# Kernel optimization log

Hardware: AMD Instinct MI355X
Metric: run time of the kernel (lower is better)

The kernel has to match this reference:

```python
import jax, jax.numpy as jnp
import numpy as np

N = 400_000
B = 64          # number of segments (point clouds)
IN_C = 128
INTER = (256, 512, 512)
OUT_C = 512


def setup_inputs() -> dict:
    key = jax.random.key(0)
    ks = jax.random.split(key, 12)
    pos_emd = jax.random.normal(ks[0], (N, IN_C), dtype=jnp.float32)
    radius_p_batch = jnp.sort(jax.random.randint(ks[1], (N,), 0, B))

    def lin(k, fin, fout):
        kw, kb = jax.random.split(k)
        s = 1.0 / np.sqrt(fin)
        W = jax.random.uniform(kw, (fin, fout), jnp.float32, -s, s)
        b = jax.random.uniform(kb, (fout,), jnp.float32, -s, s)
        return W, b

    W1, b1 = lin(ks[2], IN_C, INTER[0])
    W2, b2 = lin(ks[3], INTER[0], INTER[1])
    W3, b3 = lin(ks[4], INTER[1], INTER[2])
    W4, b4 = lin(ks[5], IN_C + INTER[2], OUT_C)
    W5, b5 = lin(ks[6], OUT_C, OUT_C)
    return {
        "pos_emd": pos_emd, "radius_p_batch": radius_p_batch,
        "W1": W1, "b1": b1, "W2": W2, "b2": b2, "W3": W3, "b3": b3,
        "W4": W4, "b4": b4, "W5": W5, "b5": b5,
    }


def reference(pos_emd, radius_p_batch, W1, b1, W2, b2, W3, b3, W4, b4, W5, b5):
    # mlp1: Linear-ReLU-Linear-ReLU-Linear
    h = jax.nn.relu(pos_emd @ W1 + b1)
    h = jax.nn.relu(h @ W2 + b2)
    h = h @ W3 + b3                              # [N, 512]
    # global max pool over segments
    g = jax.ops.segment_max(h, radius_p_batch, num_segments=B)  # [B, 512]
    # broadcast each segment's global feature back to its points (ids sorted)
    g_rep = g[radius_p_batch]                    # [N, 512]
    z = jnp.concatenate((pos_emd, g_rep), axis=-1)  # [N, 640]
    # mlp2: Linear-ReLU-Linear
    z = jax.nn.relu(z @ W4 + b4)
    z = z @ W5 + b5                              # [N, 512]
    return jax.ops.segment_max(z, radius_p_batch, num_segments=B)  # [B, 512]
```

## Files before the change

kernel.cpp:

```cpp
#include <hip/hip_runtime.h>
#include <stdint.h>


typedef __bf16 bf16;
typedef __bf16 bf16x4 __attribute__((ext_vector_type(4)));
typedef __bf16 bf16x8 __attribute__((ext_vector_type(8)));
typedef float f32x4 __attribute__((ext_vector_type(4)));
typedef __attribute__((address_space(3))) char lds_char;

#define N_PTS 400000
#define ORD_NEG_INF 0x007FFFFFu

__device__ __forceinline__ unsigned f2ord(float f) {
  unsigned u = __float_as_uint(f);
  return (u & 0x80000000u) ? ~u : (u | 0x80000000u);
}
__device__ __forceinline__ float ord2f(unsigned o) {
  unsigned u = (o & 0x80000000u) ? (o ^ 0x80000000u) : ~o;
  return __uint_as_float(u);
}

__device__ __forceinline__ void gld16(const bf16* g, lds_char* l) {
  __builtin_amdgcn_global_load_lds((const __attribute__((address_space(1))) void*)g,
                                   (__attribute__((address_space(3))) void*)l, 16, 0, 0);
}

#define DSR(dst, preg, IMM) \
  asm volatile("ds_read_b128 %0, %1 offset:%c2" : "=&v"(dst) : "v"(preg), "n"(IMM))

#define SCHED0 __builtin_amdgcn_sched_barrier(0)
#define LGKM0 do { asm volatile("s_waitcnt lgkmcnt(0)"); SCHED0; } while (0)
#define SBARR do { __builtin_amdgcn_s_barrier(); SCHED0; } while (0)
#define VMW2 do { asm volatile("s_waitcnt vmcnt(2)"); SCHED0; } while (0)
#define VMW0 do { asm volatile("s_waitcnt vmcnt(0)"); SCHED0; } while (0)

__global__ void k_init(unsigned* g_ord, unsigned* out_u) {
  int i = blockIdx.x * 256 + threadIdx.x;
  if (i < 64 * 512) { g_ord[i] = ORD_NEG_INF; out_u[i] = ORD_NEG_INF; }
}

__global__ void k_convX(const float* __restrict__ x, bf16* __restrict__ y, long n4) {
  long i = (long)blockIdx.x * 256 + threadIdx.x;
  long stride = (long)gridDim.x * 256;
  for (; i < n4; i += stride) {
    float4 v = ((const float4*)x)[i];
    bf16x4 o = {(bf16)v.x, (bf16)v.y, (bf16)v.z, (bf16)v.w};
    ((bf16x4*)y)[i] = o;
  }
}

__global__ void k_convWt(const float* __restrict__ W, bf16* __restrict__ Wt, int K, int Nout) {
  int idx = blockIdx.x * 256 + threadIdx.x;
  if (idx < K * Nout) {
    int k = idx / Nout, c = idx - k * Nout;
    Wt[(size_t)c * K + k] = (bf16)W[idx];
  }
}

__global__ void k_segbias(const unsigned* __restrict__ g_ord, const float* __restrict__ W4,
                          const float* __restrict__ b4, float* __restrict__ sb) {
  const int s = blockIdx.x, c = threadIdx.x;
  __shared__ float gs[512];
  gs[c] = ord2f(g_ord[s * 512 + c]);
  __syncthreads();
  float acc = b4[c];
  for (int j = 0; j < 512; ++j) acc = fmaf(gs[j], W4[(size_t)(128 + j) * 512 + c], acc);
  sb[s * 512 + c] = acc;
}

__global__ void k_decode(unsigned* p, int n) {
  int i = blockIdx.x * 256 + threadIdx.x;
  if (i < n) { float f = ord2f(p[i]); ((float*)p)[i] = f; }
}

template <int BIASMODE, bool RELU, int EPI, int K, int NOUT>
__launch_bounds__(512, 1)
__global__ void k_gemm(const bf16* __restrict__ A, const bf16* __restrict__ Bt,
                       const float* __restrict__ bias, const int* __restrict__ ids,
                       long row_off, bf16* __restrict__ out,
                       unsigned* __restrict__ outAtomic) {
  constexpr int NT = K / 64;
  constexpr int NIT = NT / 2;
  constexpr int NBX = NOUT / 256;
  __shared__ __align__(16) char sMem[131072];
  __shared__ int sIds[256];
  const int tid = threadIdx.x;
  const int wid = tid >> 6, lane = tid & 63;
  const int wr = wid >> 2, wc = wid & 3;
  const int lr = lane & 15, lk = lane >> 4;

  const int nwg = NBX * (int)gridDim.y;
  const int orig = (int)blockIdx.y * NBX + (int)blockIdx.x;
  const int q = nwg >> 3, r = nwg & 7;
  const int xcd = orig & 7, lid = orig >> 3;
  const int wg = (xcd < r ? xcd * (q + 1) : r * (q + 1) + (xcd - r) * q) + lid;
  const int n0 = (wg % NBX) * 256;
  const int m0 = (wg / NBX) * 256;

  if constexpr (BIASMODE == 1 || EPI == 1) {
    if (tid < 256) {
      long gi = row_off + m0 + tid;
      if (gi > (long)N_PTS - 1) gi = (long)N_PTS - 1;
      sIds[tid] = ids[gi];
    }
  }
  SCHED0;

  const int row0 = (wid * 2) * 8 + (lane >> 3);
  const int row1 = row0 + 8;
  const int sc0 = ((lane & 7) ^ (lane >> 4)) * 8;
  const int sc1 = ((lane & 7) ^ (4 + (lane >> 4))) * 8;
  lds_char* lds3 = (lds_char*)sMem;

  auto stageH = [&](int tau, int mat, int h) {
    if (tau >= NT) return;
    const int db = tau & 1;
    const bf16* srcb = (mat == 0) ? A + (size_t)(m0 + h * 128) * K
                                  : Bt + (size_t)(n0 + h * 128) * K;
    lds_char* d0 = lds3 + mat * 65536 + h * 32768 + db * 16384 + (wid * 2) * 1024;
    gld16(srcb + (size_t)row0 * K + tau * 64 + sc0, d0);
    gld16(srcb + (size_t)row1 * K + tau * 64 + sc1, d0 + 1024);
  };

  const unsigned s7 = (unsigned)(lr >> 1);
  const unsigned cks0 = (((unsigned)lk) ^ s7) * 16u;
  const unsigned cks1 = (((unsigned)lk + 4u) ^ s7) * 16u;
  lds_char* vA0 = lds3 + wr * 32768 + lr * 128 + cks0;
  lds_char* vA1 = lds3 + wr * 32768 + lr * 128 + cks1;
  lds_char* vB0 = lds3 + 65536 + (wc >> 1) * 32768 + (wc & 1) * 8192 + lr * 128 + cks0;
  lds_char* vB1 = lds3 + 65536 + (wc >> 1) * 32768 + (wc & 1) * 8192 + lr * 128 + cks1;

  bf16x8 aF[4][2], aS[4][2], bR[4][2];
  f32x4 acc[8][4];
#pragma unroll
  for (int i = 0; i < 8; ++i)
#pragma unroll
    for (int j = 0; j < 4; ++j) acc[i][j] = {0.f, 0.f, 0.f, 0.f};

#define RDA4(ARR, DB, IHI) do { \
  DSR(ARR[0][0], vA0, (DB) + ((IHI) + 0) * 2048); DSR(ARR[0][1], vA1, (DB) + ((IHI) + 0) * 2048); \
  DSR(ARR[1][0], vA0, (DB) + ((IHI) + 1) * 2048); DSR(ARR[1][1], vA1, (DB) + ((IHI) + 1) * 2048); \
  DSR(ARR[2][0], vA0, (DB) + ((IHI) + 2) * 2048); DSR(ARR[2][1], vA1, (DB) + ((IHI) + 2) * 2048); \
  DSR(ARR[3][0], vA0, (DB) + ((IHI) + 3) * 2048); DSR(ARR[3][1], vA1, (DB) + ((IHI) + 3) * 2048); \
} while (0)
#define RDB1(j, DB) \
  DSR(bR[j][0], vB0, (DB) + (j) * 2048); \
  DSR(bR[j][1], vB1, (DB) + (j) * 2048)
#define RD_B01(DB) do { RDB1(0, DB); RDB1(1, DB); } while (0)
#define RD_B23(DB) do { RDB1(2, DB); RDB1(3, DB); } while (0)
#define MMQ(AARR, II, JJ) do { __builtin_amdgcn_s_setprio(1); \
  _Pragma("unroll") for (int i_ = 0; i_ < 4; ++i_) \
  _Pragma("unroll") for (int j_ = 0; j_ < 2; ++j_) { \
    acc[(II) + i_][(JJ) + j_] = __builtin_amdgcn_mfma_f32_16x16x32_bf16(AARR[i_][0], bR[(JJ) + j_][0], acc[(II) + i_][(JJ) + j_], 0, 0, 0); \
    acc[(II) + i_][(JJ) + j_] = __builtin_amdgcn_mfma_f32_16x16x32_bf16(AARR[i_][1], bR[(JJ) + j_][1], acc[(II) + i_][(JJ) + j_], 0, 0, 0); \
  } \
  __builtin_amdgcn_s_setprio(0); } while (0)

  stageH(0, 1, 0); stageH(0, 1, 1); stageH(0, 0, 0); stageH(0, 0, 1);
  stageH(1, 1, 0);
  asm volatile("s_waitcnt vmcnt(2) lgkmcnt(0)");
  SCHED0;
  SBARR;

#pragma unroll 1
  for (int t = 0; t < NIT; ++t) {
    const int t2 = 2 * t;
    RDA4(aF, 0, 0); RD_B01(0);
    stageH(t2 + 1, 1, 1);
    SBARR; LGKM0; MMQ(aF, 0, 0);
    RD_B23(0);
    stageH(t2 + 1, 0, 0);
    SBARR; LGKM0; MMQ(aF, 0, 2);
    RDA4(aS, 0, 4);
    stageH(t2 + 1, 0, 1);
    SBARR; LGKM0; MMQ(aS, 4, 0);
    stageH(t2 + 2, 1, 0);
    MMQ(aS, 4, 2);
    if (t < NIT - 1) VMW2; else VMW0;
    SBARR;
    RDA4(aF, 16384, 0); RD_B01(16384);
    stageH(t2 + 2, 1, 1);
    SBARR; LGKM0; MMQ(aF, 0, 0);
    RD_B23(16384);
    stageH(t2 + 2, 0, 0);
    SBARR; LGKM0; MMQ(aF, 0, 2);
    RDA4(aS, 16384, 4);
    stageH(t2 + 2, 0, 1);
    SBARR; LGKM0; MMQ(aS, 4, 0);
    if (t < NIT - 1) {
      stageH(t2 + 3, 1, 0);
      MMQ(aS, 4, 2);
      VMW2; SBARR;
    } else {
      MMQ(aS, 4, 2);
    }
  }

  if constexpr (EPI == 0) {
#pragma unroll
    for (int j = 0; j < 4; ++j) {
      const int col = n0 + wc * 64 + j * 16 + lr;
      float bcol = (BIASMODE == 0) ? bias[col] : 0.f;
#pragma unroll
      for (int i = 0; i < 8; ++i) {
#pragma unroll
        for (int q2 = 0; q2 < 4; ++q2) {
          const int rl = wr * 128 + i * 16 + lk * 4 + q2;
          float v = acc[i][j][q2];
          if constexpr (BIASMODE == 0) v += bcol;
          else v += bias[(size_t)sIds[rl] * 512 + col];
          if constexpr (RELU) v = fmaxf(v, 0.f);
          out[(size_t)(m0 + rl) * NOUT + col] = (bf16)v;
        }
      }
    }
  } else {
    const int sLo = sIds[wr * 128], sHi = sIds[wr * 128 + 127];
#pragma unroll
    for (int j = 0; j < 4; ++j) {
      const int col = n0 + wc * 64 + j * 16 + lr;
      const float bcol = bias[col];
      for (int s = sLo; s <= sHi; ++s) {
        float m = -__builtin_inff();
#pragma unroll
        for (int i = 0; i < 8; ++i)
#pragma unroll
          for (int q2 = 0; q2 < 4; ++q2) {
            const int rl = wr * 128 + i * 16 + lk * 4 + q2;
            const bool rv = (row_off + m0 + rl) < (long)N_PTS;
            float v = acc[i][j][q2] + bcol;
            m = (sIds[rl] == s && rv) ? fmaxf(m, v) : m;
          }
        m = fmaxf(m, __shfl_xor(m, 16));
        m = fmaxf(m, __shfl_xor(m, 32));
        if (lane < 16) atomicMax(&outAtomic[(size_t)s * 512 + col], f2ord(m));
      }
    }
  }
#undef RDA4
#undef RDB1
#undef RD_B01
#undef RD_B23
#undef MMQ
}

static inline long lmin(long a, long b) { return a < b ? a : b; }

extern "C" void kernel_launch(void* const* d_in, const int* in_sizes, int n_in,
                              void* d_out, int out_size, void* d_ws, size_t ws_size,
                              hipStream_t stream) {
  const float* pos = (const float*)d_in[0];
  const int* ids = (const int*)d_in[1];
  const float* W1 = (const float*)d_in[2]; const float* b1 = (const float*)d_in[3];
  const float* W2 = (const float*)d_in[4]; const float* b2 = (const float*)d_in[5];
  const float* W3 = (const float*)d_in[6]; const float* b3 = (const float*)d_in[7];
  const float* W4 = (const float*)d_in[8]; const float* b4 = (const float*)d_in[9];
  const float* W5 = (const float*)d_in[10]; const float* b5 = (const float*)d_in[11];

  char* ws = (char*)d_ws;
  size_t off = 0;
  auto alloc = [&](size_t bytes) -> char* {
    off = (off + 255) & ~(size_t)255;
    char* p = ws + off; off += bytes; return p;
  };
  bf16* Wt1  = (bf16*)alloc(128 * 256 * 2);
  bf16* Wt2  = (bf16*)alloc(256 * 512 * 2);
  bf16* Wt3  = (bf16*)alloc(512 * 512 * 2);
  bf16* Wt4a = (bf16*)alloc(128 * 512 * 2);
  bf16* Wt5  = (bf16*)alloc(512 * 512 * 2);
  unsigned* g_ord = (unsigned*)alloc(64 * 512 * 4);
  float* sb = (float*)alloc(64 * 512 * 4);
  bf16* Xbf = (bf16*)alloc((size_t)(N_PTS + 384) * 128 * 2);

  const size_t per_row = (256 + 512) * 2;
  size_t fixed_end = (off + 255) & ~(size_t)255;
  long avail = (long)ws_size - (long)fixed_end - 8192;
  long maxrows = avail / (long)per_row;
  long chunk = (maxrows - 256) & ~255L;
  if (chunk > N_PTS) chunk = N_PTS;
  if (chunk < 256) chunk = 256;
  long rows_alloc = chunk + 256;

  bf16* h1 = (bf16*)alloc((size_t)rows_alloc * 256 * 2);
  bf16* h2 = (bf16*)alloc((size_t)rows_alloc * 512 * 2);

  k_init<<<dim3(128), dim3(256), 0, stream>>>(g_ord, (unsigned*)d_out);
  k_convWt<<<dim3((128 * 256 + 255) / 256), dim3(256), 0, stream>>>(W1, Wt1, 128, 256);
  k_convWt<<<dim3((256 * 512 + 255) / 256), dim3(256), 0, stream>>>(W2, Wt2, 256, 512);
  k_convWt<<<dim3((512 * 512 + 255) / 256), dim3(256), 0, stream>>>(W3, Wt3, 512, 512);
  k_convWt<<<dim3((128 * 512 + 255) / 256), dim3(256), 0, stream>>>(W4, Wt4a, 128, 512);
  k_convWt<<<dim3((512 * 512 + 255) / 256), dim3(256), 0, stream>>>(W5, Wt5, 512, 512);
  k_convX<<<dim3(2048), dim3(256), 0, stream>>>(pos, Xbf, (long)N_PTS * 32);

  for (long o = 0; o < N_PTS; o += chunk) {
    long rows = lmin(chunk, N_PTS - o);
    unsigned mb = (unsigned)((rows + 255) / 256);
    k_gemm<0, true, 0, 128, 256><<<dim3(1, mb), dim3(512), 0, stream>>>(Xbf + o * 128, Wt1, b1, ids, o, h1, nullptr);
    k_gemm<0, true, 0, 256, 512><<<dim3(2, mb), dim3(512), 0, stream>>>(h1, Wt2, b2, ids, o, h2, nullptr);
    k_gemm<0, false, 1, 512, 512><<<dim3(2, mb), dim3(512), 0, stream>>>(h2, Wt3, b3, ids, o, nullptr, g_ord);
  }
  k_segbias<<<dim3(64), dim3(512), 0, stream>>>(g_ord, W4, b4, sb);
  for (long o = 0; o < N_PTS; o += chunk) {
    long rows = lmin(chunk, N_PTS - o);
    unsigned mb = (unsigned)((rows + 255) / 256);
    k_gemm<1, true, 0, 128, 512><<<dim3(2, mb), dim3(512), 0, stream>>>(Xbf + o * 128, Wt4a, sb, ids, o, h2, nullptr);
    k_gemm<0, false, 1, 512, 512><<<dim3(2, mb), dim3(512), 0, stream>>>(h2, Wt5, b5, ids, o, nullptr, (unsigned*)d_out);
  }
  k_decode<<<dim3(128), dim3(256), 0, stream>>>((unsigned*)d_out, 64 * 512);
}
```

Baseline: 1.103 ms.

## Restructure GEMM main loop into 4-stage BK=32 LDS pipeline with single barrier

After: 1.155 ms. +4.8%, slower.

```diff
diff --git a/kernel.cpp b/kernel.cpp
--- a/kernel.cpp
+++ b/kernel.cpp
@@ -30,8 +30,10 @@
 
 #define SCHED0 __builtin_amdgcn_sched_barrier(0)
 #define LGKM0 do { asm volatile("s_waitcnt lgkmcnt(0)"); SCHED0; } while (0)
+#define LGKM4 do { asm volatile("s_waitcnt lgkmcnt(4)"); SCHED0; } while (0)
 #define SBARR do { __builtin_amdgcn_s_barrier(); SCHED0; } while (0)
-#define VMW2 do { asm volatile("s_waitcnt vmcnt(2)"); SCHED0; } while (0)
+#define VMW8 do { asm volatile("s_waitcnt vmcnt(8)"); SCHED0; } while (0)
+#define VMW4 do { asm volatile("s_waitcnt vmcnt(4)"); SCHED0; } while (0)
 #define VMW0 do { asm volatile("s_waitcnt vmcnt(0)"); SCHED0; } while (0)
 
 __global__ void k_init(unsigned* g_ord, unsigned* out_u) {
@@ -74,13 +76,12 @@
 }
 
 template <int BIASMODE, bool RELU, int EPI, int K, int NOUT>
-__launch_bounds__(512, 1)
+__launch_bounds__(512, 2)
 __global__ void k_gemm(const bf16* __restrict__ A, const bf16* __restrict__ Bt,
                        const float* __restrict__ bias, const int* __restrict__ ids,
                        long row_off, bf16* __restrict__ out,
                        unsigned* __restrict__ outAtomic) {
-  constexpr int NT = K / 64;
-  constexpr int NIT = NT / 2;
+  constexpr int NT = K / 32;
   constexpr int NBX = NOUT / 256;
   __shared__ __align__(16) char sMem[131072];
   __shared__ int sIds[256];
@@ -106,95 +107,72 @@
   }
   SCHED0;
 
-  const int row0 = (wid * 2) * 8 + (lane >> 3);
-  const int row1 = row0 + 8;
-  const int sc0 = ((lane & 7) ^ (lane >> 4)) * 8;
-  const int sc1 = ((lane & 7) ^ (4 + (lane >> 4))) * 8;
   lds_char* lds3 = (lds_char*)sMem;
 
-  auto stageH = [&](int tau, int mat, int h) {
-    if (tau >= NT) return;
-    const int db = tau & 1;
-    const bf16* srcb = (mat == 0) ? A + (size_t)(m0 + h * 128) * K
-                                  : Bt + (size_t)(n0 + h * 128) * K;
-    lds_char* d0 = lds3 + mat * 65536 + h * 32768 + db * 16384 + (wid * 2) * 1024;
-    gld16(srcb + (size_t)row0 * K + tau * 64 + sc0, d0);
-    gld16(srcb + (size_t)row1 * K + tau * 64 + sc1, d0 + 1024);
+  const int hg = wid >> 1;
+  const bf16* hbase = (hg < 2) ? (A + (size_t)(m0 + (hg & 1) * 128) * K)
+                               : (Bt + (size_t)(n0 + (hg & 1) * 128) * K);
+  const int rIn = lane >> 2;
+  const int cblk = ((lane & 3) ^ ((lane >> 3) & 3)) * 8;
+  const bf16* srcP[4];
+  lds_char* dstP[4];
+#pragma unroll
+  for (int k = 0; k < 4; ++k) {
+    const int s8 = (wid & 1) * 4 + k;
+    srcP[k] = hbase + (size_t)(s8 * 16 + rIn) * K + cblk;
+    dstP[k] = lds3 + hg * 8192 + s8 * 1024 + lane * 16;
+  }
+  auto STG = [&](int tau) {
+    if (tau < NT) {
+      const int bo = (tau & 3) << 15;
+      const int ko = tau * 32;
+#pragma unroll
+      for (int k = 0; k < 4; ++k) gld16(srcP[k] + ko, dstP[k] + bo);
+    }
   };
 
-  const unsigned s7 = (unsigned)(lr >> 1);
-  const unsigned cks0 = (((unsigned)lk) ^ s7) * 16u;
-  const unsigned cks1 = (((unsigned)lk + 4u) ^ s7) * 16u;
-  lds_char* vA0 = lds3 + wr * 32768 + lr * 128 + cks0;
-  lds_char* vA1 = lds3 + wr * 32768 + lr * 128 + cks1;
-  lds_char* vB0 = lds3 + 65536 + (wc >> 1) * 32768 + (wc & 1) * 8192 + lr * 128 + cks0;
-  lds_char* vB1 = lds3 + 65536 + (wc >> 1) * 32768 + (wc & 1) * 8192 + lr * 128 + cks1;
-
-  bf16x8 aF[4][2], aS[4][2], bR[4][2];
+  const unsigned sl16 = (((unsigned)lk) ^ ((unsigned)(lr >> 1) & 3u)) * 16u;
+  lds_char* vA = lds3 + wr * 8192 + lr * 64 + sl16;
+  lds_char* vB = lds3 + 16384 + (wc >> 1) * 8192 + (wc & 1) * 4096 + lr * 64 + sl16;
+
+  bf16x8 aR[8], bR[4];
   f32x4 acc[8][4];
 #pragma unroll
   for (int i = 0; i < 8; ++i)
 #pragma unroll
     for (int j = 0; j < 4; ++j) acc[i][j] = {0.f, 0.f, 0.f, 0.f};
 
-#define RDA4(ARR, DB, IHI) do { \
-  DSR(ARR[0][0], vA0, (DB) + ((IHI) + 0) * 2048); DSR(ARR[0][1], vA1, (DB) + ((IHI) + 0) * 2048); \
-  DSR(ARR[1][0], vA0, (DB) + ((IHI) + 1) * 2048); DSR(ARR[1][1], vA1, (DB) + ((IHI) + 1) * 2048); \
-  DSR(ARR[2][0], vA0, (DB) + ((IHI) + 2) * 2048); DSR(ARR[2][1], vA1, (DB) + ((IHI) + 2) * 2048); \
-  DSR(ARR[3][0], vA0, (DB) + ((IHI) + 3) * 2048); DSR(ARR[3][1], vA1, (DB) + ((IHI) + 3) * 2048); \
-} while (0)
-#define RDB1(j, DB) \
-  DSR(bR[j][0], vB0, (DB) + (j) * 2048); \
-  DSR(bR[j][1], vB1, (DB) + (j) * 2048)
-#define RD_B01(DB) do { RDB1(0, DB); RDB1(1, DB); } while (0)
-#define RD_B23(DB) do { RDB1(2, DB); RDB1(3, DB); } while (0)
-#define MMQ(AARR, II, JJ) do { __builtin_amdgcn_s_setprio(1); \
+#define MM8(ILO) do { __builtin_amdgcn_s_setprio(1); \
   _Pragma("unroll") for (int i_ = 0; i_ < 4; ++i_) \
-  _Pragma("unroll") for (int j_ = 0; j_ < 2; ++j_) { \
-    acc[(II) + i_][(JJ) + j_] = __builtin_amdgcn_mfma_f32_16x16x32_bf16(AARR[i_][0], bR[(JJ) + j_][0], acc[(II) + i_][(JJ) + j_], 0, 0, 0); \
-    acc[(II) + i_][(JJ) + j_] = __builtin_amdgcn_mfma_f32_16x16x32_bf16(AARR[i_][1], bR[(JJ) + j_][1], acc[(II) + i_][(JJ) + j_], 0, 0, 0); \
-  } \
+  _Pragma("unroll") for (int j_ = 0; j_ < 4; ++j_) \
+    acc[(ILO) + i_][j_] = __builtin_amdgcn_mfma_f32_16x16x32_bf16(aR[(ILO) + i_], bR[j_], acc[(ILO) + i_][j_], 0, 0, 0); \
   __builtin_amdgcn_s_setprio(0); } while (0)
 
-  stageH(0, 1, 0); stageH(0, 1, 1); stageH(0, 0, 0); stageH(0, 0, 1);
-  stageH(1, 1, 0);
-  asm volatile("s_waitcnt vmcnt(2) lgkmcnt(0)");
+  STG(0); STG(1); STG(2);
+  asm volatile("s_waitcnt vmcnt(8) lgkmcnt(0)");
   SCHED0;
   SBARR;
 
 #pragma unroll 1
-  for (int t = 0; t < NIT; ++t) {
-    const int t2 = 2 * t;
-    RDA4(aF, 0, 0); RD_B01(0);
-    stageH(t2 + 1, 1, 1);
-    SBARR; LGKM0; MMQ(aF, 0, 0);
-    RD_B23(0);
-    stageH(t2 + 1, 0, 0);
-    SBARR; LGKM0; MMQ(aF, 0, 2);
-    RDA4(aS, 0, 4);
-    stageH(t2 + 1, 0, 1);
-    SBARR; LGKM0; MMQ(aS, 4, 0);
-    stageH(t2 + 2, 1, 0);
-    MMQ(aS, 4, 2);
-    if (t < NIT - 1) VMW2; else VMW0;
-    SBARR;
-    RDA4(aF, 16384, 0); RD_B01(16384);
-    stageH(t2 + 2, 1, 1);
-    SBARR; LGKM0; MMQ(aF, 0, 0);
-    RD_B23(16384);
-    stageH(t2 + 2, 0, 0);
-    SBARR; LGKM0; MMQ(aF, 0, 2);
-    RDA4(aS, 16384, 4);
-    stageH(t2 + 2, 0, 1);
-    SBARR; LGKM0; MMQ(aS, 4, 0);
-    if (t < NIT - 1) {
-      stageH(t2 + 3, 1, 0);
-      MMQ(aS, 4, 2);
-      VMW2; SBARR;
-    } else {
-      MMQ(aS, 4, 2);
-    }
-  }
+  for (int t = 0; t < NT; ++t) {
+    lds_char* pA = vA + ((t & 3) << 15);
+    lds_char* pB = vB + ((t & 3) << 15);
+    DSR(bR[0], pB, 0); DSR(bR[1], pB, 1024); DSR(bR[2], pB, 2048); DSR(bR[3], pB, 3072);
+    DSR(aR[0], pA, 0); DSR(aR[1], pA, 1024); DSR(aR[2], pA, 2048); DSR(aR[3], pA, 3072);
+    DSR(aR[4], pA, 4096); DSR(aR[5], pA, 5120); DSR(aR[6], pA, 6144); DSR(aR[7], pA, 7168);
+    STG(t + 3);
+    LGKM4;
+    MM8(0);
+    LGKM0;
+    MM8(4);
+    if (t < NT - 1) {
+      if (t + 3 < NT) VMW8;
+      else if (t + 2 < NT) VMW4;
+      else VMW0;
+      SBARR;
+    }
+  }
+#undef MM8
 
   if constexpr (EPI == 0) {
 #pragma unroll
@@ -237,11 +215,6 @@
       }
     }
   }
-#undef RDA4
-#undef RDB1
-#undef RD_B01
-#undef RD_B23
-#undef MMQ
 }
 
 static inline long lmin(long a, long b) { return a < b ? a : b; }
```
